# Performance work log

Hardware: AMD Instinct MI355X
Metric: run time of the kernel (lower is better)

The kernel has to match this reference:

```python
import jax, jax.numpy as jnp
import numpy as np

D_MODEL = 512
NUM_EXPERTS = 8
TOP_K = 2
FFN = 2048
H = 2 * D_MODEL            # GRU hidden per direction
GRU_OUT = 4 * D_MODEL      # bidirectional concat
B, T = 8, 1024
BAL_W, Z_W = 0.01, 0.001


def setup_inputs() -> dict:
    key = jax.random.key(0)
    ks = jax.random.split(key, 12)
    s = 1.0 / np.sqrt(H)  # torch GRU uniform init scale
    u = lambda k, shape: jax.random.uniform(k, shape, jnp.float32, -s, s)
    tn = lambda k, shape: jax.random.normal(k, shape, jnp.float32) * 0.02
    return {
        "x": jax.random.normal(ks[0], (B, T, D_MODEL), jnp.float32),
        # GRU params, stacked [2 directions, ...]; gate order (r, z, n) as in torch
        "gru_Wih": u(ks[1], (2, 3 * H, D_MODEL)),
        "gru_Whh": u(ks[2], (2, 3 * H, H)),
        "gru_bih": u(ks[3], (2, 3 * H)),
        "gru_bhh": u(ks[4], (2, 3 * H)),
        "gate_W": tn(ks[5], (NUM_EXPERTS, GRU_OUT)),
        "gate_b": jnp.zeros((NUM_EXPERTS,), jnp.float32),
        "W1": tn(ks[6], (NUM_EXPERTS, GRU_OUT, FFN)),
        "b1": jnp.zeros((NUM_EXPERTS, FFN), jnp.float32),
        "W2": tn(ks[7], (NUM_EXPERTS, FFN, D_MODEL)),
        "b2": jnp.zeros((NUM_EXPERTS, D_MODEL), jnp.float32),
    }


def _gru_bidir(x, Wih, Whh, bih, bhh):
    # x: [B,T,D]; returns [B,T,2H]
    Bn = x.shape[0]

    def run(d, reverse):
        # precompute input projections: [T,B,3H]
        xg = jnp.swapaxes(jnp.einsum('btd,gd->btg', x, Wih[d]) + bih[d], 0, 1)
        Whh_d, bhh_d = Whh[d], bhh[d]

        def step(h, xt):
            hg = h @ Whh_d.T + bhh_d
            xr, xz, xn = jnp.split(xt, 3, axis=-1)
            hr, hz, hn = jnp.split(hg, 3, axis=-1)
            r = jax.nn.sigmoid(xr + hr)
            z = jax.nn.sigmoid(xz + hz)
            n = jnp.tanh(xn + r * hn)
            h_new = (1.0 - z) * n + z * h
            return h_new, h_new

        h0 = jnp.zeros((Bn, H), x.dtype)
        _, ys = jax.lax.scan(step, h0, xg, reverse=reverse)  # ys[t] aligned with time t
        return jnp.swapaxes(ys, 0, 1)

    return jnp.concatenate([run(0, False), run(1, True)], axis=-1)


def reference(x, gru_Wih, gru_Whh, gru_bih, gru_bhh, gate_W, gate_b, W1, b1, W2, b2):
    Bn, Tn, _ = x.shape
    n = Bn * Tn
    E = NUM_EXPERTS

    gru_out = _gru_bidir(x, gru_Wih, gru_Whh, gru_bih, gru_bhh)
    gru_out = jax.nn.leaky_relu(gru_out, 0.01)          # dropout=0.0 -> identity
    flat = gru_out.reshape(n, GRU_OUT)

    # gating (expert_bias buffer is zeros at init)
    logits = flat @ gate_W.T + gate_b                    # [n,E]
    z_loss = Z_W * jnp.mean(jnp.square(jax.nn.logsumexp(logits, axis=-1)))
    scores = jax.nn.softmax(logits, axis=-1)
    top_scores, top_idx = jax.lax.top_k(scores, TOP_K)   # [n,K]
    weights = top_scores / jnp.sum(top_scores, axis=-1, keepdims=True)

    expert_mask = jnp.sum(jax.nn.one_hot(top_idx, E, dtype=jnp.float32), axis=1)  # [n,E]
    f = jax.lax.stop_gradient(jnp.mean(expert_mask, axis=0))
    P = jnp.mean(scores, axis=0)
    balance_loss = BAL_W * E * jnp.sum(f * P)
    aux_loss = balance_loss + z_loss

    # masked-dense expert combine (math identical to gather/scatter loop)
    output = jnp.zeros((n, D_MODEL), jnp.float32)
    for e in range(E):
        h = jax.nn.gelu(flat @ W1[e] + b1[e], approximate=False)  # [n,FFN]
        out_e = h @ W2[e] + b2[e]                                 # [n,D]
        w_e = jnp.sum(weights * (top_idx == e), axis=-1)          # [n]
        output = output + w_e[:, None] * out_e

    return output.reshape(Bn, Tn, D_MODEL).astype(x.dtype), aux_loss
```

## Files before the change

### kernel.cpp

```cpp
#include <hip/hip_runtime.h>
#include <math.h>

#define NTOK 8192
#define DM   512
#define HID  1024
#define G3H  3072
#define GOUT 2048
#define FFND 2048
#define NEXP 8

typedef float f32x4 __attribute__((ext_vector_type(4)));

#define XG_OFF    0ULL
#define HG_OFF    0ULL
#define OG_OFF    134217728ULL
#define FLAT_OFF  201326592ULL
#define HBUF_OFF  268435456ULL
#define FLAGS_OFF 268566528ULL
#define IMETA_OFF 268567552ULL
#define FMETA_OFF 268571648ULL
#define TKIDX_OFF 268575744ULL
#define TKW_OFF   268641280ULL
#define PAIRT_OFF 268706816ULL
#define PAIRW_OFF 268772352ULL
#define SLOT_OFF  268837888ULL

__global__ void k0_init(unsigned* p) {
    int i = blockIdx.x * 256 + threadIdx.x;
    if (i < 32768) p[i] = (unsigned)((i >> 13) & 1);
    else if (i < 35072) p[i] = 0u;
}

__global__ __launch_bounds__(256, 2) void k1_sgemm_bt(
    const float* __restrict__ A, const float* __restrict__ B,
    const float* __restrict__ bias, float* __restrict__ C) {
    __shared__ float As[16 * 132];
    __shared__ float Bs[16 * 132];
    const int tid = threadIdx.x;
    const int m0 = blockIdx.y * 128;
    const int n0 = blockIdx.x * 128;
    const int tx = tid & 15, ty = tid >> 4;
    const int arow = tid >> 2, ac4 = (tid & 3) * 4;
    float acc[8][8];
#pragma unroll
    for (int i = 0; i < 8; ++i)
#pragma unroll
        for (int j = 0; j < 8; ++j) acc[i][j] = 0.f;

    for (int k0 = 0; k0 < 512; k0 += 16) {
        __syncthreads();
#pragma unroll
        for (int r = 0; r < 2; ++r) {
            int row = r * 64 + arow;
            float4 va = *(const float4*)(A + (size_t)(m0 + row) * 512 + k0 + ac4);
            As[(ac4 + 0) * 132 + row] = va.x;
            As[(ac4 + 1) * 132 + row] = va.y;
            As[(ac4 + 2) * 132 + row] = va.z;
            As[(ac4 + 3) * 132 + row] = va.w;
            float4 vb = *(const float4*)(B + (size_t)(n0 + row) * 512 + k0 + ac4);
            Bs[(ac4 + 0) * 132 + row] = vb.x;
            Bs[(ac4 + 1) * 132 + row] = vb.y;
            Bs[(ac4 + 2) * 132 + row] = vb.z;
            Bs[(ac4 + 3) * 132 + row] = vb.w;
        }
        __syncthreads();
#pragma unroll
        for (int k = 0; k < 16; ++k) {
            float4 a0 = *(const float4*)&As[k * 132 + ty * 8];
            float4 a1 = *(const float4*)&As[k * 132 + ty * 8 + 4];
            float4 b0 = *(const float4*)&Bs[k * 132 + tx * 8];
            float4 b1 = *(const float4*)&Bs[k * 132 + tx * 8 + 4];
            float av[8] = {a0.x, a0.y, a0.z, a0.w, a1.x, a1.y, a1.z, a1.w};
            float bv[8] = {b0.x, b0.y, b0.z, b0.w, b1.x, b1.y, b1.z, b1.w};
#pragma unroll
            for (int i = 0; i < 8; ++i)
#pragma unroll
                for (int j = 0; j < 8; ++j) acc[i][j] = fmaf(av[i], bv[j], acc[i][j]);
        }
    }
    float4 c0 = *(const float4*)(bias + n0 + tx * 8);
    float4 c1 = *(const float4*)(bias + n0 + tx * 8 + 4);
    float bb[8] = {c0.x, c0.y, c0.z, c0.w, c1.x, c1.y, c1.z, c1.w};
#pragma unroll
    for (int i = 0; i < 8; ++i) {
        float* op = C + (size_t)(m0 + ty * 8 + i) * 6144 + n0 + tx * 8;
        float4 o0 = make_float4(acc[i][0] + bb[0], acc[i][1] + bb[1],
                                acc[i][2] + bb[2], acc[i][3] + bb[3]);
        float4 o1 = make_float4(acc[i][4] + bb[4], acc[i][5] + bb[5],
                                acc[i][6] + bb[6], acc[i][7] + bb[7]);
        *(float4*)op = o0;
        *(float4*)(op + 4) = o1;
    }
}

__global__ __launch_bounds__(256) void k2_gru(
    const float* __restrict__ Whh, const float* __restrict__ bhh,
    const float* __restrict__ xg, float* __restrict__ flat,
    float* hbuf) {
    __shared__ float hlsf[8192];
    __shared__ float red[64 * 196];
    __shared__ float s2b[192];
    char* hls = (char*)hlsf;
    const int tid = threadIdx.x;
    const int dir = blockIdx.x >> 7;
    const int wg = blockIdx.x & 127;
    const int j0 = wg << 3;
    float* hb = hbuf + dir * 16384;
    const int rg = tid >> 6;
    const int kc = tid & 63;
    const int swz = (kc & 7) << 4;
    const int lane = tid & 63;

    const float* W0 = Whh + (size_t)dir * G3H * HID;
    float wreg[6][16];
#pragma unroll
    for (int rr = 0; rr < 6; ++rr) {
        const int r = rg * 6 + rr;
        const float* wp = W0 + (size_t)(((r >> 3) << 10) + j0 + (r & 7)) * 1024 + (kc << 4);
        const float4 w0 = ((const float4*)wp)[0];
        const float4 w1 = ((const float4*)wp)[1];
        const float4 w2 = ((const float4*)wp)[2];
        const float4 w3 = ((const float4*)wp)[3];
        wreg[rr][0] = w0.x;  wreg[rr][1] = w0.y;  wreg[rr][2] = w0.z;  wreg[rr][3] = w0.w;
        wreg[rr][4] = w1.x;  wreg[rr][5] = w1.y;  wreg[rr][6] = w1.z;  wreg[rr][7] = w1.w;
        wreg[rr][8] = w2.x;  wreg[rr][9] = w2.y;  wreg[rr][10] = w2.z; wreg[rr][11] = w2.w;
        wreg[rr][12] = w3.x; wreg[rr][13] = w3.y; wreg[rr][14] = w3.z; wreg[rr][15] = w3.w;
    }
    float bhh_r = 0.f;
    if (tid < 192) {
        const int r = tid >> 3;
        bhh_r = bhh[dir * G3H + ((r >> 3) << 10) + j0 + (r & 7)];
    }
    const int u = tid >> 3, bb = tid & 7;
    const int wswz = ((tid >> 5) & 7) << 4;
    float hprev = 0.f;

    for (int s = 1; s <= 1024; ++s) {
        const int te = dir ? (1024 - s) : (s - 1);
        float xr = 0.f, xz = 0.f, xn = 0.f;
        if (tid < 64) {
            const float* xp = xg + (size_t)((bb << 10) + te) * 6144 + dir * G3H + j0 + u;
            xr = xp[0];
            xz = xp[1024];
            xn = xp[2048];
        }
        const float* hp = hb + (((s - 1) & 1) << 13);
        const unsigned expb = (((unsigned)(s - 1)) >> 1) & 1u;
        if (s > 1) {
            int it = 0;
            for (;;) {
                float a = __hip_atomic_load(hp + (lane << 6) + 17,
                                            __ATOMIC_RELAXED, __HIP_MEMORY_SCOPE_AGENT);
                float b = __hip_atomic_load(hp + 4096 + (lane << 6) + 17,
                                            __ATOMIC_RELAXED, __HIP_MEMORY_SCOPE_AGENT);
                bool ok = ((__float_as_uint(a) & 1u) == expb) &&
                          ((__float_as_uint(b) & 1u) == expb);
                if (__all(ok)) break;
                if (++it > (1 << 22)) break;
                __builtin_amdgcn_s_sleep(1);
            }
        }
        const float* hbase = hp + (tid << 2);
        f32x4 hv4[8];
        {
            int it2 = 0;
            for (;;) {
#pragma unroll
                for (int c = 0; c < 8; ++c)
                    asm volatile("global_load_dwordx4 %0, %1, off sc0 sc1"
                                 : "=v"(hv4[c]) : "v"(hbase + (c << 10)));
                asm volatile("s_waitcnt vmcnt(0)" ::: "memory");
                __builtin_amdgcn_sched_barrier(0);
                bool ok = true;
#pragma unroll
                for (int c = 0; c < 8; ++c) {
                    ok = ok && ((__float_as_uint(hv4[c].x) & 1u) == expb)
                            && ((__float_as_uint(hv4[c].y) & 1u) == expb)
                            && ((__float_as_uint(hv4[c].z) & 1u) == expb)
                            && ((__float_as_uint(hv4[c].w) & 1u) == expb);
                }
                if (__all(ok)) break;
                if (++it2 > (1 << 18)) break;
            }
        }
#pragma unroll
        for (int c = 0; c < 8; ++c) {
            const int off = ((c << 12) + (tid << 4)) ^ wswz;
            *(f32x4*)(hls + off) = hv4[c];
        }
        __syncthreads();
        float acc[6][8];
#pragma unroll
        for (int rr = 0; rr < 6; ++rr)
#pragma unroll
            for (int q = 0; q < 8; ++q) acc[rr][q] = 0.f;
#pragma unroll
        for (int i = 0; i < 16; ++i) {
            const int kbase = ((kc << 4) + i) << 5;
            const float4 hA = *(const float4*)(hls + (kbase ^ swz));
            const float4 hB = *(const float4*)(hls + ((kbase + 16) ^ swz));
#pragma unroll
            for (int rr = 0; rr < 6; ++rr) {
                const float w = wreg[rr][i];
                acc[rr][0] = fmaf(w, hA.x, acc[rr][0]);
                acc[rr][1] = fmaf(w, hA.y, acc[rr][1]);
                acc[rr][2] = fmaf(w, hA.z, acc[rr][2]);
                acc[rr][3] = fmaf(w, hA.w, acc[rr][3]);
                acc[rr][4] = fmaf(w, hB.x, acc[rr][4]);
                acc[rr][5] = fmaf(w, hB.y, acc[rr][5]);
                acc[rr][6] = fmaf(w, hB.z, acc[rr][6]);
                acc[rr][7] = fmaf(w, hB.w, acc[rr][7]);
            }
        }
        float* rp = red + kc * 196 + rg * 48;
#pragma unroll
        for (int rr = 0; rr < 6; ++rr) {
            *(float4*)(rp + (rr << 3)) =
                make_float4(acc[rr][0], acc[rr][1], acc[rr][2], acc[rr][3]);
            *(float4*)(rp + (rr << 3) + 4) =
                make_float4(acc[rr][4], acc[rr][5], acc[rr][6], acc[rr][7]);
        }
        __syncthreads();
        if (tid < 192) {
            float a0 = 0.f, a1 = 0.f, a2 = 0.f, a3 = 0.f;
#pragma unroll
            for (int q = 0; q < 64; q += 4) {
                a0 += red[(q + 0) * 196 + tid];
                a1 += red[(q + 1) * 196 + tid];
                a2 += red[(q + 2) * 196 + tid];
                a3 += red[(q + 3) * 196 + tid];
            }
            s2b[tid] = (a0 + a1) + (a2 + a3) + bhh_r;
        }
        __syncthreads();
        if (tid < 64) {
            const float hr = s2b[tid];
            const float hz = s2b[64 + tid];
            const float hn = s2b[128 + tid];
            const float rg_ = 1.f / (1.f + expf(-(xr + hr)));
            const float zg_ = 1.f / (1.f + expf(-(xz + hz)));
            const float ng_ = tanhf(xn + rg_ * hn);
            const float hnew = (1.f - zg_) * ng_ + zg_ * hprev;
            hprev = hnew;
            const unsigned hu = (__float_as_uint(hnew) & ~1u) | (((unsigned)s >> 1) & 1u);
            __hip_atomic_store(hb + ((s & 1) << 13) + ((j0 + u) << 3) + bb,
                               __uint_as_float(hu),
                               __ATOMIC_RELAXED, __HIP_MEMORY_SCOPE_AGENT);
            const float lr = hnew > 0.f ? hnew : 0.01f * hnew;
            flat[(size_t)((bb << 10) + te) * 2048 + dir * 1024 + j0 + u] = lr;
        }
    }
}

__global__ __launch_bounds__(256) void k3_gate(
    const float* __restrict__ flat, const float* __restrict__ gate_W,
    const float* __restrict__ gate_b,
    int* __restrict__ tk_idx, float* __restrict__ tk_w,
    int* __restrict__ counts, float* __restrict__ fmeta) {
    __shared__ float gw[8 * 2048];
    __shared__ float bP[9];
    __shared__ int bC[8];
    const int tid = threadIdx.x;
    for (int i = tid; i < 8 * 2048; i += 256) gw[i] = gate_W[i];
    if (tid < 9) bP[tid] = 0.f;
    if (tid < 8) bC[tid] = 0;
    __syncthreads();
    const int lane = tid & 63, w = tid >> 6;
    const int tbase = blockIdx.x * 16 + w * 4;
    for (int j = 0; j < 4; ++j) {
        int t = tbase + j;
        const float* fr = flat + (size_t)t * 2048;
        float a[8];
#pragma unroll
        for (int e = 0; e < 8; ++e) a[e] = 0.f;
        for (int i = 0; i < 32; ++i) {
            float v = fr[i * 64 + lane];
#pragma unroll
            for (int e = 0; e < 8; ++e) a[e] = fmaf(v, gw[e * 2048 + i * 64 + lane], a[e]);
        }
#pragma unroll
        for (int e = 0; e < 8; ++e) {
#pragma unroll
            for (int off = 32; off > 0; off >>= 1) a[e] += __shfl_down(a[e], off);
        }
        if (lane == 0) {
            float lg[8];
#pragma unroll
            for (int e = 0; e < 8; ++e) lg[e] = a[e] + gate_b[e];
            float m = lg[0];
#pragma unroll
            for (int e = 1; e < 8; ++e) m = fmaxf(m, lg[e]);
            float sc[8], ssum = 0.f;
#pragma unroll
            for (int e = 0; e < 8; ++e) { sc[e] = expf(lg[e] - m); ssum += sc[e]; }
            float inv = 1.f / ssum;
#pragma unroll
            for (int e = 0; e < 8; ++e) sc[e] *= inv;
            float lse = m + logf(ssum);
            int i1 = 0; float s1 = sc[0];
#pragma unroll
            for (int e = 1; e < 8; ++e) if (sc[e] > s1) { s1 = sc[e]; i1 = e; }
            int i2 = (i1 == 0) ? 1 : 0; float s2v = sc[i2];
#pragma unroll
            for (int e = 0; e < 8; ++e) if (e != i1 && sc[e] > s2v) { s2v = sc[e]; i2 = e; }
            float wsum = s1 + s2v;
            tk_idx[2 * t] = i1; tk_idx[2 * t + 1] = i2;
            tk_w[2 * t] = s1 / wsum; tk_w[2 * t + 1] = s2v / wsum;
            atomicAdd(&bC[i1], 1);
            atomicAdd(&bC[i2], 1);
#pragma unroll
            for (int e = 0; e < 8; ++e) atomicAdd(&bP[e], sc[e]);
            atomicAdd(&bP[8], lse * lse);
        }
    }
    __syncthreads();
    if (tid < 8) {
        atomicAdd(&counts[tid], bC[tid]);
        atomicAdd(&fmeta[tid], bP[tid]);
    }
    if (tid == 8) atomicAdd(&fmeta[8], bP[8]);
}

__global__ void k4_sched(int* im, float* fm, float* aux_out) {
    int tid = threadIdx.x;
    if (tid < 136) { im[32 + tid] = -1; im[168 + tid] = 0; }
    __syncthreads();
    if (tid == 0) {
        int off = 0;
        for (int e = 0; e < 8; ++e) { im[16 + e] = off; im[8 + e] = off; off += im[e]; }
        im[24] = off;
        int T = 0;
        for (int e = 0; e < 8; ++e) {
            int c = im[e], o = im[16 + e];
            for (int i = 0; i < c; i += 128) { im[32 + T] = e; im[168 + T] = o + i; ++T; }
        }
        im[25] = T;
        float fP = 0.f;
        for (int e = 0; e < 8; ++e) fP += ((float)im[e] / 8192.f) * (fm[e] / 8192.f);
        *aux_out = 0.01f * 8.f * fP + 0.001f * (fm[8] / 8192.f);
    }
}

__global__ __launch_bounds__(256) void k5_scatter(
    const int* __restrict__ tk_idx, const float* __restrict__ tk_w,
    int* __restrict__ im, int* __restrict__ pair_t,
    float* __restrict__ pair_w, int* __restrict__ slot) {
    __shared__ int cnt[8], base[8];
    const int tid = threadIdx.x;
    if (tid < 8) cnt[tid] = 0;
    __syncthreads();
    const int t = blockIdx.x * 256 + tid;
    const int e0 = tk_idx[2 * t], e1 = tk_idx[2 * t + 1];
    const int p0 = atomicAdd(&cnt[e0], 1);
    const int p1 = atomicAdd(&cnt[e1], 1);
    __syncthreads();
    if (tid < 8) base[tid] = atomicAdd(&im[8 + tid], cnt[tid]);
    __syncthreads();
    const int q0 = base[e0] + p0, q1 = base[e1] + p1;
    pair_t[q0] = t; pair_w[q0] = tk_w[2 * t];     slot[2 * t] = q0;
    pair_t[q1] = t; pair_w[q1] = tk_w[2 * t + 1]; slot[2 * t + 1] = q1;
}

__global__ __launch_bounds__(256, 2) void k6_ffn1(
    const float* __restrict__ flat, const float* __restrict__ W1,
    const float* __restrict__ b1, const int* __restrict__ im,
    const int* __restrict__ pair_t, float* __restrict__ Hg) {
    const int rt = blockIdx.x % 136;
    const int nt = blockIdx.x / 136;
    const int e = im[32 + rt];
    if (e < 0) return;
    const int pStart = im[168 + rt];
    const int pEnd = im[16 + e + 1];
    __shared__ float As[16 * 132];
    __shared__ float Bs[16 * 132];
    const int tid = threadIdx.x;
    const int tx = tid & 15, ty = tid >> 4;
    const int n0 = nt * 128;
    const float* Bb = W1 + (size_t)e * 2048 * 2048;
    const int arow = tid >> 2, ac4 = (tid & 3) * 4;
    const int bk = tid >> 4, bn = (tid & 15) * 8;
    int r0 = pStart + arow;       if (r0 > pEnd - 1) r0 = pEnd - 1;
    int r1 = pStart + 64 + arow;  if (r1 > pEnd - 1) r1 = pEnd - 1;
    const float* arp0 = flat + (size_t)pair_t[r0] * 2048;
    const float* arp1 = flat + (size_t)pair_t[r1] * 2048;
    float acc[8][8];
#pragma unroll
    for (int i = 0; i < 8; ++i)
#pragma unroll
        for (int j = 0; j < 8; ++j) acc[i][j] = 0.f;

    for (int k0 = 0; k0 < 2048; k0 += 16) {
        __syncthreads();
        {
            float4 va = *(const float4*)(arp0 + k0 + ac4);
            As[(ac4 + 0) * 132 + arow] = va.x;
            As[(ac4 + 1) * 132 + arow] = va.y;
            As[(ac4 + 2) * 132 + arow] = va.z;
            As[(ac4 + 3) * 132 + arow] = va.w;
            float4 vb = *(const float4*)(arp1 + k0 + ac4);
            As[(ac4 + 0) * 132 + 64 + arow] = vb.x;
            As[(ac4 + 1) * 132 + 64 + arow] = vb.y;
            As[(ac4 + 2) * 132 + 64 + arow] = vb.z;
            As[(ac4 + 3) * 132 + 64 + arow] = vb.w;
            float4 w0 = *(const float4*)(Bb + (size_t)(k0 + bk) * 2048 + n0 + bn);
            float4 w1 = *(const float4*)(Bb + (size_t)(k0 + bk) * 2048 + n0 + bn + 4);
            *(float4*)&Bs[bk * 132 + bn] = w0;
            *(float4*)&Bs[bk * 132 + bn + 4] = w1;
        }
        __syncthreads();
#pragma unroll
        for (int k = 0; k < 16; ++k) {
            float4 a0 = *(const float4*)&As[k * 132 + ty * 8];
            float4 a1 = *(const float4*)&As[k * 132 + ty * 8 + 4];
            float4 b0 = *(const float4*)&Bs[k * 132 + tx * 8];
            float4 b1v = *(const float4*)&Bs[k * 132 + tx * 8 + 4];
            float av[8] = {a0.x, a0.y, a0.z, a0.w, a1.x, a1.y, a1.z, a1.w};
            float bv[8] = {b0.x, b0.y, b0.z, b0.w, b1v.x, b1v.y, b1v.z, b1v.w};
#pragma unroll
            for (int i = 0; i < 8; ++i)
#pragma unroll
                for (int j = 0; j < 8; ++j) acc[i][j] = fmaf(av[i], bv[j], acc[i][j]);
        }
    }
    float4 c0 = *(const float4*)(b1 + (size_t)e * 2048 + n0 + tx * 8);
    float4 c1 = *(const float4*)(b1 + (size_t)e * 2048 + n0 + tx * 8 + 4);
    float bb[8] = {c0.x, c0.y, c0.z, c0.w, c1.x, c1.y, c1.z, c1.w};
#pragma unroll
    for (int i = 0; i < 8; ++i) {
        int p = pStart + ty * 8 + i;
        if (p < pEnd) {
            float* op = Hg + (size_t)p * 2048 + n0 + tx * 8;
            float o[8];
#pragma unroll
            for (int j = 0; j < 8; ++j) {
                float xv = acc[i][j] + bb[j];
                o[j] = 0.5f * xv * (1.f + erff(xv * 0.70710678118654752f));
            }
            *(float4*)op = make_float4(o[0], o[1], o[2], o[3]);
            *(float4*)(op + 4) = make_float4(o[4], o[5], o[6], o[7]);
        }
    }
}

__global__ __launch_bounds__(256, 2) void k7_ffn2(
    const float* __restrict__ Hg, const float* __restrict__ W2,
    const float* __restrict__ b2, const int* __restrict__ im,
    float* __restrict__ Og) {
    const int rt = blockIdx.x % 136;
    const int nt = blockIdx.x / 136;
    const int e = im[32 + rt];
    if (e < 0) return;
    const int pStart = im[168 + rt];
    const int pEnd = im[16 + e + 1];
    __shared__ float As[16 * 132];
    __shared__ float Bs[16 * 132];
    const int tid = threadIdx.x;
    const int tx = tid & 15, ty = tid >> 4;
    const int n0 = nt * 128;
    const float* Bb = W2 + (size_t)e * 2048 * 512;
    const int arow = tid >> 2, ac4 = (tid & 3) * 4;
    const int bk = tid >> 4, bn = (tid & 15) * 8;
    int r0 = pStart + arow;       if (r0 > pEnd - 1) r0 = pEnd - 1;
    int r1 = pStart + 64 + arow;  if (r1 > pEnd - 1) r1 = pEnd - 1;
    const float* arp0 = Hg + (size_t)r0 * 2048;
    const float* arp1 = Hg + (size_t)r1 * 2048;
    float acc[8][8];
#pragma unroll
    for (int i = 0; i < 8; ++i)
#pragma unroll
        for (int j = 0; j < 8; ++j) acc[i][j] = 0.f;

    for (int k0 = 0; k0 < 2048; k0 += 16) {
        __syncthreads();
        {
            float4 va = *(const float4*)(arp0 + k0 + ac4);
            As[(ac4 + 0) * 132 + arow] = va.x;
            As[(ac4 + 1) * 132 + arow] = va.y;
            As[(ac4 + 2) * 132 + arow] = va.z;
            As[(ac4 + 3) * 132 + arow] = va.w;
            float4 vb = *(const float4*)(arp1 + k0 + ac4);
            As[(ac4 + 0) * 132 + 64 + arow] = vb.x;
            As[(ac4 + 1) * 132 + 64 + arow] = vb.y;
            As[(ac4 + 2) * 132 + 64 + arow] = vb.z;
            As[(ac4 + 3) * 132 + 64 + arow] = vb.w;
            float4 w0 = *(const float4*)(Bb + (size_t)(k0 + bk) * 512 + n0 + bn);
            float4 w1 = *(const float4*)(Bb + (size_t)(k0 + bk) * 512 + n0 + bn + 4);
            *(float4*)&Bs[bk * 132 + bn] = w0;
            *(float4*)&Bs[bk * 132 + bn + 4] = w1;
        }
        __syncthreads();
#pragma unroll
        for (int k = 0; k < 16; ++k) {
            float4 a0 = *(const float4*)&As[k * 132 + ty * 8];
            float4 a1 = *(const float4*)&As[k * 132 + ty * 8 + 4];
            float4 b0 = *(const float4*)&Bs[k * 132 + tx * 8];
            float4 b1v = *(const float4*)&Bs[k * 132 + tx * 8 + 4];
            float av[8] = {a0.x, a0.y, a0.z, a0.w, a1.x, a1.y, a1.z, a1.w};
            float bv[8] = {b0.x, b0.y, b0.z, b0.w, b1v.x, b1v.y, b1v.z, b1v.w};
#pragma unroll
            for (int i = 0; i < 8; ++i)
#pragma unroll
                for (int j = 0; j < 8; ++j) acc[i][j] = fmaf(av[i], bv[j], acc[i][j]);
        }
    }
    float4 c0 = *(const float4*)(b2 + (size_t)e * 512 + n0 + tx * 8);
    float4 c1 = *(const float4*)(b2 + (size_t)e * 512 + n0 + tx * 8 + 4);
    float bb[8] = {c0.x, c0.y, c0.z, c0.w, c1.x, c1.y, c1.z, c1.w};
#pragma unroll
    for (int i = 0; i < 8; ++i) {
        int p = pStart + ty * 8 + i;
        if (p < pEnd) {
            float* op = Og + (size_t)p * 512 + n0 + tx * 8;
            *(float4*)op = make_float4(acc[i][0] + bb[0], acc[i][1] + bb[1],
                                       acc[i][2] + bb[2], acc[i][3] + bb[3]);
            *(float4*)(op + 4) = make_float4(acc[i][4] + bb[4], acc[i][5] + bb[5],
                                             acc[i][6] + bb[6], acc[i][7] + bb[7]);
        }
    }
}

__global__ __launch_bounds__(256) void k8_comb(
    const float* __restrict__ Og, const int* __restrict__ slot,
    const float* __restrict__ pw, float* __restrict__ out) {
    const int i4 = blockIdx.x * 256 + threadIdx.x;
    const int t = i4 >> 7;
    const int d = (i4 & 127) << 2;
    const int s0 = slot[2 * t], s1 = slot[2 * t + 1];
    const float w0 = pw[s0], w1 = pw[s1];
    float4 a = *(const float4*)(Og + (size_t)s0 * 512 + d);
    float4 b = *(const float4*)(Og + (size_t)s1 * 512 + d);
    float4 o = make_float4(w0 * a.x + w1 * b.x, w0 * a.y + w1 * b.y,
                           w0 * a.z + w1 * b.z, w0 * a.w + w1 * b.w);
    *(float4*)(out + (size_t)t * 512 + d) = o;
}

extern "C" void kernel_launch(void* const* d_in, const int* in_sizes, int n_in,
                              void* d_out, int out_size, void* d_ws, size_t ws_size,
                              hipStream_t stream) {
    (void)in_sizes; (void)n_in; (void)out_size; (void)ws_size;
    const float* x   = (const float*)d_in[0];
    const float* Wih = (const float*)d_in[1];
    const float* Whh = (const float*)d_in[2];
    const float* bih = (const float*)d_in[3];
    const float* bhh = (const float*)d_in[4];
    const float* gW  = (const float*)d_in[5];
    const float* gb  = (const float*)d_in[6];
    const float* W1  = (const float*)d_in[7];
    const float* b1  = (const float*)d_in[8];
    const float* W2  = (const float*)d_in[9];
    const float* b2  = (const float*)d_in[10];
    float* out = (float*)d_out;
    char* ws = (char*)d_ws;
    float* xg    = (float*)(ws + XG_OFF);
    float* Hg    = (float*)(ws + HG_OFF);
    float* Og    = (float*)(ws + OG_OFF);
    float* flat  = (float*)(ws + FLAT_OFF);
    float* hbuf  = (float*)(ws + HBUF_OFF);
    int*   im    = (int*)(ws + IMETA_OFF);
    float* fm    = (float*)(ws + FMETA_OFF);
    int*   tki   = (int*)(ws + TKIDX_OFF);
    float* tkw   = (float*)(ws + TKW_OFF);
    int*   prt   = (int*)(ws + PAIRT_OFF);
    float* prw   = (float*)(ws + PAIRW_OFF);
    int*   slt   = (int*)(ws + SLOT_OFF);

    hipLaunchKernelGGL(k0_init, dim3(138), dim3(256), 0, stream, (unsigned*)(ws + HBUF_OFF));
    hipLaunchKernelGGL(k1_sgemm_bt, dim3(48, 64), dim3(256), 0, stream, x, Wih, bih, xg);
    hipLaunchKernelGGL(k2_gru, dim3(256), dim3(256), 0, stream, Whh, bhh, xg, flat, hbuf);
    hipLaunchKernelGGL(k3_gate, dim3(512), dim3(256), 0, stream, flat, gW, gb, tki, tkw, im, fm);
    hipLaunchKernelGGL(k4_sched, dim3(1), dim3(256), 0, stream, im, fm, out + 4194304);
    hipLaunchKernelGGL(k5_scatter, dim3(32), dim3(256), 0, stream, tki, tkw, im, prt, prw, slt);
    hipLaunchKernelGGL(k6_ffn1, dim3(136 * 16), dim3(256), 0, stream, flat, W1, b1, im, prt, Hg);
    hipLaunchKernelGGL(k7_ffn2, dim3(136 * 4), dim3(256), 0, stream, Hg, W2, b2, im, Og);
    hipLaunchKernelGGL(k8_comb, dim3(4096), dim3(256), 0, stream, Og, slt, prw, out);
}
```

Before: 9.558 ms.

## Use per-workgroup step flags and wave-local h loads in GRU recurrence

The persistent GRU kernel now has each workgroup publish a step counter flag, and waiters poll 32 flags per wave instead of sampling parity bits in the hidden-state buffer. The thread-to-(row,k) mapping is changed so each wave loads only the h slice it consumes, which lets the block-wide barrier before the matvec become a wave-local LDS wait. This aims to cut grid-synchronisation latency on the sequential critical path of 1024 steps. The risks are that flags are written with relaxed ordering by one thread, possibly before other lanes' h stores are visible, and that the flags buffer must be reset between calls.

```diff
diff --git a/kernel.cpp b/kernel.cpp
--- a/kernel.cpp
+++ b/kernel.cpp
@@ -96,7 +96,7 @@
 __global__ __launch_bounds__(256) void k2_gru(
     const float* __restrict__ Whh, const float* __restrict__ bhh,
     const float* __restrict__ xg, float* __restrict__ flat,
-    float* hbuf) {
+    float* hbuf, int* flags) {
     __shared__ float hlsf[8192];
     __shared__ float red[64 * 196];
     __shared__ float s2b[192];
@@ -106,10 +106,12 @@
     const int wg = blockIdx.x & 127;
     const int j0 = wg << 3;
     float* hb = hbuf + dir * 16384;
-    const int rg = tid >> 6;
-    const int kc = tid & 63;
-    const int swz = (kc & 7) << 4;
+    int* fl = flags + dir * 128;
+    const int rg = tid & 3;
+    const int kc = tid >> 2;
+    const int wv = tid >> 6;
     const int lane = tid & 63;
+    const int xr16 = (kc & 15) << 4;
 
     const float* W0 = Whh + (size_t)dir * G3H * HID;
     float wreg[6][16];
@@ -132,7 +134,6 @@
         bhh_r = bhh[dir * G3H + ((r >> 3) << 10) + j0 + (r & 7)];
     }
     const int u = tid >> 3, bb = tid & 7;
-    const int wswz = ((tid >> 5) & 7) << 4;
     float hprev = 0.f;
 
     for (int s = 1; s <= 1024; ++s) {
@@ -147,20 +148,18 @@
         const float* hp = hb + (((s - 1) & 1) << 13);
         const unsigned expb = (((unsigned)(s - 1)) >> 1) & 1u;
         if (s > 1) {
+            const int c0 = s - 1;
             int it = 0;
             for (;;) {
-                float a = __hip_atomic_load(hp + (lane << 6) + 17,
-                                            __ATOMIC_RELAXED, __HIP_MEMORY_SCOPE_AGENT);
-                float b = __hip_atomic_load(hp + 4096 + (lane << 6) + 17,
-                                            __ATOMIC_RELAXED, __HIP_MEMORY_SCOPE_AGENT);
-                bool ok = ((__float_as_uint(a) & 1u) == expb) &&
-                          ((__float_as_uint(b) & 1u) == expb);
-                if (__all(ok)) break;
-                if (++it > (1 << 22)) break;
+                int f = __hip_atomic_load(fl + (wv << 5) + (lane & 31),
+                                          __ATOMIC_RELAXED, __HIP_MEMORY_SCOPE_AGENT);
+                if (__all(f >= c0)) break;
+                if (++it > (1 << 20)) break;
                 __builtin_amdgcn_s_sleep(1);
             }
         }
-        const float* hbase = hp + (tid << 2);
+        asm volatile("" ::: "memory");
+        const float* hbase = hp + (wv << 11) + (lane << 2);
         f32x4 hv4[8];
         {
             int it2 = 0;
@@ -168,27 +167,31 @@
 #pragma unroll
                 for (int c = 0; c < 8; ++c)
                     asm volatile("global_load_dwordx4 %0, %1, off sc0 sc1"
-                                 : "=v"(hv4[c]) : "v"(hbase + (c << 10)));
+                                 : "=v"(hv4[c]) : "v"(hbase + (c << 8)));
                 asm volatile("s_waitcnt vmcnt(0)" ::: "memory");
                 __builtin_amdgcn_sched_barrier(0);
-                bool ok = true;
+                unsigned bad = 0u;
 #pragma unroll
                 for (int c = 0; c < 8; ++c) {
-                    ok = ok && ((__float_as_uint(hv4[c].x) & 1u) == expb)
-                            && ((__float_as_uint(hv4[c].y) & 1u) == expb)
-                            && ((__float_as_uint(hv4[c].z) & 1u) == expb)
-                            && ((__float_as_uint(hv4[c].w) & 1u) == expb);
+                    bad |= (__float_as_uint(hv4[c].x) ^ expb);
+                    bad |= (__float_as_uint(hv4[c].y) ^ expb);
+                    bad |= (__float_as_uint(hv4[c].z) ^ expb);
+                    bad |= (__float_as_uint(hv4[c].w) ^ expb);
                 }
-                if (__all(ok)) break;
-                if (++it2 > (1 << 18)) break;
+                if (__all((bad & 1u) == 0u)) break;
+                if (++it2 > (1 << 16)) break;
+                __builtin_amdgcn_s_sleep(1);
             }
         }
 #pragma unroll
         for (int c = 0; c < 8; ++c) {
-            const int off = ((c << 12) + (tid << 4)) ^ wswz;
+            const int off = (wv << 13) +
+                ((((c << 10) + (lane << 4))) ^ ((((c << 1) | (lane >> 5)) & 15) << 4));
             *(f32x4*)(hls + off) = hv4[c];
         }
-        __syncthreads();
+        asm volatile("s_waitcnt lgkmcnt(0)" ::: "memory");
+        __builtin_amdgcn_sched_barrier(0);
+        const int rbase = wv << 13;
         float acc[6][8];
 #pragma unroll
         for (int rr = 0; rr < 6; ++rr)
@@ -196,9 +199,10 @@
             for (int q = 0; q < 8; ++q) acc[rr][q] = 0.f;
 #pragma unroll
         for (int i = 0; i < 16; ++i) {
-            const int kbase = ((kc << 4) + i) << 5;
-            const float4 hA = *(const float4*)(hls + (kbase ^ swz));
-            const float4 hB = *(const float4*)(hls + ((kbase + 16) ^ swz));
+            const int k_local = ((kc & 15) << 4) + i;
+            const int a0 = rbase + ((k_local << 5) ^ xr16);
+            const float4 hA = *(const float4*)(hls + a0);
+            const float4 hB = *(const float4*)(hls + (a0 ^ 16));
 #pragma unroll
             for (int rr = 0; rr < 6; ++rr) {
                 const float w = wreg[rr][i];
@@ -246,6 +250,9 @@
             __hip_atomic_store(hb + ((s & 1) << 13) + ((j0 + u) << 3) + bb,
                                __uint_as_float(hu),
                                __ATOMIC_RELAXED, __HIP_MEMORY_SCOPE_AGENT);
+            asm volatile("" ::: "memory");
+            if (tid == 0)
+                __hip_atomic_store(fl + wg, s, __ATOMIC_RELAXED, __HIP_MEMORY_SCOPE_AGENT);
             const float lr = hnew > 0.f ? hnew : 0.01f * hnew;
             flat[(size_t)((bb << 10) + te) * 2048 + dir * 1024 + j0 + u] = lr;
         }
@@ -556,6 +563,7 @@
     float* Og    = (float*)(ws + OG_OFF);
     float* flat  = (float*)(ws + FLAT_OFF);
     float* hbuf  = (float*)(ws + HBUF_OFF);
+    int*   flags = (int*)(ws + FLAGS_OFF);
     int*   im    = (int*)(ws + IMETA_OFF);
     float* fm    = (float*)(ws + FMETA_OFF);
     int*   tki   = (int*)(ws + TKIDX_OFF);
@@ -566,7 +574,7 @@
 
     hipLaunchKernelGGL(k0_init, dim3(138), dim3(256), 0, stream, (unsigned*)(ws + HBUF_OFF));
     hipLaunchKernelGGL(k1_sgemm_bt, dim3(48, 64), dim3(256), 0, stream, x, Wih, bih, xg);
-    hipLaunchKernelGGL(k2_gru, dim3(256), dim3(256), 0, stream, Whh, bhh, xg, flat, hbuf);
+    hipLaunchKernelGGL(k2_gru, dim3(256), dim3(256), 0, stream, Whh, bhh, xg, flat, hbuf, flags);
     hipLaunchKernelGGL(k3_gate, dim3(512), dim3(256), 0, stream, flat, gW, gb, tki, tkw, im, fm);
     hipLaunchKernelGGL(k4_sched, dim3(1), dim3(256), 0, stream, im, fm, out + 4194304);
     hipLaunchKernelGGL(k5_scatter, dim3(32), dim3(256), 0, stream, tki, tkw, im, prt, prw, slt);
```

After: 9.998 ms. +4.6%, slower.
